# Optimization experiments

Hardware: AMD Instinct MI355X
Metric: run time of the kernel (lower is better)

## Reference

```python
import jax, jax.numpy as jnp
import numpy as np

HIDDEN = 1024
N_HEADS = 16
HEAD_DIM = HIDDEN // N_HEADS  # 64


def setup_inputs() -> dict:
    key = jax.random.key(0)
    ks = jax.random.split(key, 5)
    B, S = 4, 4096
    x = jax.random.normal(ks[0], (B, S, HIDDEN), dtype=jnp.float32)
    scale = 1.0 / np.sqrt(HIDDEN)
    wq = jax.random.normal(ks[1], (HIDDEN, HIDDEN), dtype=jnp.float32) * scale
    wk = jax.random.normal(ks[2], (HIDDEN, HIDDEN), dtype=jnp.float32) * scale
    wv = jax.random.normal(ks[3], (HIDDEN, HIDDEN), dtype=jnp.float32) * scale
    wo = jax.random.normal(ks[4], (HIDDEN, HIDDEN), dtype=jnp.float32) * scale
    return {"x": x, "wq": wq, "wk": wk, "wv": wv, "wo": wo}


def reference(x, wq, wk, wv, wo):
    # Weights stored as (out, in) like torch nn.Linear; y = x @ W^T
    B, S, H = x.shape
    q = (x @ wq.T).reshape(B, S, N_HEADS, HEAD_DIM)
    k = (x @ wk.T).reshape(B, S, N_HEADS, HEAD_DIM)
    v = (x @ wv.T).reshape(B, S, N_HEADS, HEAD_DIM)
    # Faithful to original: no transpose to (B,H,S,D) -> scores are over HEADS
    # attn: (B, S, H_heads, H_heads)
    attn = jnp.einsum("bshd,bsgd->bshg", q, k) / np.sqrt(HEAD_DIM)
    attn = jax.nn.softmax(attn, axis=-1)
    out = jnp.einsum("bshg,bsgd->bshd", attn, v).reshape(B, S, H)
    return out @ wo.T
```

## Files before the change

### kernel.cpp

```cpp
#include <hip/hip_runtime.h>
#include <hip/hip_bf16.h>


typedef __bf16 bf16;
typedef __attribute__((ext_vector_type(8))) __bf16 bf16x8;
typedef __attribute__((ext_vector_type(4))) float floatx4;

#define HIDDEN 1024
#define BM 128
#define BN 128
#define BK 32

#define VMCNT(N) asm volatile("s_waitcnt vmcnt(" #N ")" ::: "memory")
#define LGKM0()                                                                \
    do {                                                                       \
        asm volatile("s_waitcnt lgkmcnt(0)" ::: "memory");                     \
        __builtin_amdgcn_sched_barrier(0);                                     \
    } while (0)
#define SBAR() __builtin_amdgcn_s_barrier()

__device__ __forceinline__ void async_load16(const bf16* g, bf16* lds) {
    __builtin_amdgcn_global_load_lds(
        (const __attribute__((address_space(1))) void*)g,
        (__attribute__((address_space(3))) void*)lds, 16, 0, 0);
}

__device__ __forceinline__ bf16x8 load8(const bf16* p) {
    return *(const bf16x8*)p;
}
__device__ __forceinline__ bf16x8 load8(const float* p) {
    floatx4 lo = *(const floatx4*)p;
    floatx4 hi = *(const floatx4*)(p + 4);
    bf16x8 r;
#pragma unroll
    for (int i = 0; i < 4; ++i) { r[i] = (bf16)lo[i]; r[i + 4] = (bf16)hi[i]; }
    return r;
}

__global__ __launch_bounds__(256) void cvt_all(
    const float* __restrict__ x,
    const float* __restrict__ wq, const float* __restrict__ wk,
    const float* __restrict__ wv, const float* __restrict__ wo,
    bf16* __restrict__ xb, bf16* __restrict__ wpk, int mh8)
{
    const int per = (HIDDEN * HIDDEN) / 8;
    int i = blockIdx.x * 256 + threadIdx.x;
    if (i < mh8) {
        *(bf16x8*)&xb[(size_t)i * 8] = load8(&x[(size_t)i * 8]);
    } else {
        int j = i - mh8;
        int wsel = j / per;
        int off  = (j - wsel * per) * 8;
        const float* s = wsel == 0 ? wq : wsel == 1 ? wk : wsel == 2 ? wv : wo;
        *(bf16x8*)&wpk[(size_t)j * 8] = load8(&s[off]);
    }
}


template <int S>
__device__ __forceinline__ void stage_half(const bf16* __restrict__ gbase,
                                           int ld, int kt, bf16* lhalf,
                                           int h, int tid) {
#pragma unroll
    for (int j = 0; j < 2; ++j) {
        const int ci = j * 512 + tid;
        const int rr = ci >> 3;
        const int cs = (ci & 7) ^ (rr & 7);
        const int gr = h * S + (rr & (S - 1)) + (rr >> (S == 64 ? 6 : 5)) * (2 * S);
        async_load16(&gbase[(size_t)gr * ld + kt + cs * 8], &lhalf[ci * 8]);
    }
}

__device__ __forceinline__ void ld_a4(const bf16* h, int wm, int col, int quad,
                                      int cx, bf16x8* a) {
#pragma unroll
    for (int i = 0; i < 4; ++i) {
        const int rr = i * 16 + col + (wm << 6);
#pragma unroll
        for (int kk = 0; kk < 2; ++kk)
            a[i * 2 + kk] =
                *(const bf16x8*)&h[rr * 64 + (((kk << 2) + quad) ^ cx) * 8];
    }
}
__device__ __forceinline__ void ld_b2(const bf16* h, int wn, int col, int quad,
                                      int cx, bf16x8* b) {
#pragma unroll
    for (int j = 0; j < 2; ++j) {
        const int rr = j * 16 + col + (wn << 5);
#pragma unroll
        for (int kk = 0; kk < 2; ++kk)
            b[j * 2 + kk] =
                *(const bf16x8*)&h[rr * 64 + (((kk << 2) + quad) ^ cx) * 8];
    }
}

template <int H, int G>
__device__ __forceinline__ void mmq(floatx4 (&acc)[8][4], const bf16x8 (&a)[8],
                                    const bf16x8 (&bb)[4]) {
    __builtin_amdgcn_s_setprio(1);
#pragma unroll
    for (int i = 0; i < 4; ++i)
#pragma unroll
        for (int j = 0; j < 2; ++j)
#pragma unroll
            for (int kk = 0; kk < 2; ++kk)
                acc[H * 4 + i][G * 2 + j] =
                    __builtin_amdgcn_mfma_f32_16x16x32_bf16(
                        a[i * 2 + kk], bb[j * 2 + kk],
                        acc[H * 4 + i][G * 2 + j], 0, 0, 0);
    __builtin_amdgcn_s_setprio(0);
}

template <typename TC>
__global__ __launch_bounds__(512, 2) void gemm8p(
    const bf16* __restrict__ A, const bf16* __restrict__ W,
    TC* __restrict__ C, int K, int lda, int ldc)
{
    __shared__ __align__(16) bf16 sA[2][2][128 * 64];
    __shared__ __align__(16) bf16 sB[2][2][128 * 64];

    const int tid  = threadIdx.x;
    const int lane = tid & 63;
    const int w    = tid >> 6;
    const int wm   = w >> 2;
    const int wn   = w & 3;
    const int col  = lane & 15;
    const int quad = lane >> 4;
    const int cx   = col & 7;

    const int gx = gridDim.x, gy = gridDim.y;
    const int nwg = gx * gy;
    int lin = blockIdx.y * gx + blockIdx.x;
    if ((nwg & 7) == 0) {
        const int cpx = nwg >> 3;
        lin = (lin & 7) * cpx + (lin >> 3);
    }
    const int m0 = (lin / gy) * 256;
    const int n0 = (lin % gy) * 256;

    const bf16* Ab = A + (size_t)m0 * lda;
    const bf16* Wb = W + (size_t)n0 * K;

    floatx4 acc[8][4] = {};
    bf16x8 a[8], b0[4], b1[4];

    const int T = K / 64;

    stage_half<64>(Ab, lda, 0, sA[0][0], 0, tid);
    stage_half<32>(Wb, K,   0, sB[0][0], 0, tid);
    stage_half<32>(Wb, K,   0, sB[0][1], 1, tid);
    stage_half<64>(Ab, lda, 0, sA[0][1], 1, tid);
    if (T > 1) {
        stage_half<64>(Ab, lda, 64, sA[1][0], 0, tid);
        stage_half<32>(Wb, K,   64, sB[1][0], 0, tid);
        stage_half<32>(Wb, K,   64, sB[1][1], 1, tid);
        VMCNT(6);
    } else {
        VMCNT(0);
    }
    SBAR();

    for (int t = 0; t < T; ++t) {
        const int b = t & 1;

        ld_a4(sA[b][0], wm, col, quad, cx, a);
        ld_b2(sB[b][0], wn, col, quad, cx, b0);
        if (t + 1 < T) stage_half<64>(Ab, lda, (t + 1) * 64, sA[b ^ 1][1], 1, tid);
        SBAR();
        LGKM0();
        mmq<0, 0>(acc, a, b0);
        SBAR();

        ld_b2(sB[b][1], wn, col, quad, cx, b1);
        SBAR();
        LGKM0();
        mmq<0, 1>(acc, a, b1);
        SBAR();

        ld_a4(sA[b][1], wm, col, quad, cx, a);
        if (t + 2 < T) {
            stage_half<64>(Ab, lda, (t + 2) * 64, sA[b][0], 0, tid);
            stage_half<32>(Wb, K,   (t + 2) * 64, sB[b][0], 0, tid);
        }
        SBAR();
        LGKM0();
        mmq<1, 1>(acc, a, b1);
        SBAR();

        if (t + 2 < T) {
            stage_half<32>(Wb, K, (t + 2) * 64, sB[b][1], 1, tid);
            VMCNT(6);
        } else {
            VMCNT(0);
        }
        SBAR();
        LGKM0();
        mmq<1, 0>(acc, a, b0);
        SBAR();
    }

#pragma unroll
    for (int mi = 0; mi < 8; ++mi) {
#pragma unroll
        for (int r = 0; r < 4; ++r) {
            const int row = m0 + wm * 128 + mi * 16 + quad * 4 + r;
#pragma unroll
            for (int ni = 0; ni < 4; ++ni) {
                const int cc = n0 + wn * 64 + ni * 16 + col;
                C[(size_t)row * ldc + cc] = (TC)acc[mi][ni][r];
            }
        }
    }
}

template <typename TA, typename TB, typename TC>
__global__ __launch_bounds__(256, 2) void gemm_bt(
    const TA* __restrict__ A, const TB* __restrict__ W,
    TC* __restrict__ C, int M, int N, int K)
{
    __shared__ __align__(16) bf16 sA[BM * BK];
    __shared__ __align__(16) bf16 sB[BN * BK];

    const int tid  = threadIdx.x;
    const int lane = tid & 63;
    const int w    = tid >> 6;
    const int wm   = w >> 1;
    const int wn   = w & 1;
    const int m0   = blockIdx.x * BM;
    const int n0   = blockIdx.y * BN;
    const int col  = lane & 15;
    const int quad = lane >> 4;

    floatx4 acc[4][4] = {};

    for (int kt = 0; kt < K; kt += BK) {
        bf16x8 ga[2], gb[2];
#pragma unroll
        for (int i = 0; i < 2; ++i) {
            const int c   = i * 256 + tid;
            const int row = c >> 2;
            const int kc  = c & 3;
            ga[i] = load8(&A[(size_t)(m0 + row) * K + kt + kc * 8]);
            gb[i] = load8(&W[(size_t)(n0 + row) * K + kt + kc * 8]);
        }
        __syncthreads();
#pragma unroll
        for (int i = 0; i < 2; ++i) {
            const int c = i * 256 + tid;
            *(bf16x8*)&sA[c * 8] = ga[i];
            *(bf16x8*)&sB[c * 8] = gb[i];
        }
        __syncthreads();

        bf16x8 af[4], bfr[4];
#pragma unroll
        for (int mi = 0; mi < 4; ++mi)
            af[mi] = *(const bf16x8*)&sA[(wm * 64 + mi * 16 + col) * BK + quad * 8];
#pragma unroll
        for (int ni = 0; ni < 4; ++ni)
            bfr[ni] = *(const bf16x8*)&sB[(wn * 64 + ni * 16 + col) * BK + quad * 8];

#pragma unroll
        for (int mi = 0; mi < 4; ++mi)
#pragma unroll
            for (int ni = 0; ni < 4; ++ni)
                acc[mi][ni] = __builtin_amdgcn_mfma_f32_16x16x32_bf16(
                    af[mi], bfr[ni], acc[mi][ni], 0, 0, 0);
    }

#pragma unroll
    for (int mi = 0; mi < 4; ++mi) {
#pragma unroll
        for (int r = 0; r < 4; ++r) {
            const int row = m0 + wm * 64 + mi * 16 + quad * 4 + r;
#pragma unroll
            for (int ni = 0; ni < 4; ++ni) {
                const int cc = n0 + wn * 64 + ni * 16 + col;
                C[(size_t)row * N + cc] = (TC)acc[mi][ni][r];
            }
        }
    }
}

__global__ __launch_bounds__(256) void attn_heads(
    bf16* base, size_t koff, size_t voff, int stride, bf16* ob)
{
    __shared__ __align__(16) bf16 sP[4][16 * 40];

    const int tid   = threadIdx.x;
    const int lane  = tid & 63;
    const int w     = tid >> 6;
    const int token = blockIdx.x * 4 + w;
    const int col   = lane & 15;
    const int quad  = lane >> 4;

    bf16* qt = base + (size_t)token * stride;
    const bf16* kt = qt + koff;
    const bf16* vt = qt + voff;
    bf16* ot = ob + (size_t)token * HIDDEN;

    bf16x8 vb[4] = {};
    if (quad < 2) {
#pragma unroll
        for (int dt = 0; dt < 4; ++dt)
#pragma unroll
            for (int j = 0; j < 8; ++j)
                vb[dt][j] = vt[(quad * 8 + j) * 64 + dt * 16 + col];
    }

    bf16x8 qa0 = *(const bf16x8*)&qt[col * 64 + quad * 8];
    bf16x8 qa1 = *(const bf16x8*)&qt[col * 64 + 32 + quad * 8];
    bf16x8 kb0 = *(const bf16x8*)&kt[col * 64 + quad * 8];
    bf16x8 kb1 = *(const bf16x8*)&kt[col * 64 + 32 + quad * 8];
    floatx4 s = {};
    s = __builtin_amdgcn_mfma_f32_16x16x32_bf16(qa0, kb0, s, 0, 0, 0);
    s = __builtin_amdgcn_mfma_f32_16x16x32_bf16(qa1, kb1, s, 0, 0, 0);

#pragma unroll
    for (int r = 0; r < 4; ++r) {
        float e = __expf(s[r] * 0.125f);
        float su = e;
#pragma unroll
        for (int off = 1; off < 16; off <<= 1)
            su += __shfl_xor(su, off);
        sP[w][(quad * 4 + r) * 40 + col] = (bf16)(e / su);
    }

    bf16x8 pa = {};
    if (quad < 2) pa = *(const bf16x8*)&sP[w][col * 40 + quad * 8];
#pragma unroll
    for (int dt = 0; dt < 4; ++dt) {
        floatx4 o4 = {};
        o4 = __builtin_amdgcn_mfma_f32_16x16x32_bf16(pa, vb[dt], o4, 0, 0, 0);
#pragma unroll
        for (int r = 0; r < 4; ++r)
            ot[(quad * 4 + r) * 64 + dt * 16 + col] = (bf16)o4[r];
    }
}

extern "C" void kernel_launch(void* const* d_in, const int* in_sizes, int n_in,
                              void* d_out, int out_size, void* d_ws, size_t ws_size,
                              hipStream_t stream) {
    const float* x  = (const float*)d_in[0];
    const float* wq = (const float*)d_in[1];
    const float* wk = (const float*)d_in[2];
    const float* wv = (const float*)d_in[3];
    const float* wo = (const float*)d_in[4];
    float* out = (float*)d_out;

    const int M = in_sizes[0] / HIDDEN;
    const size_t MH = (size_t)M * HIDDEN;
    const size_t WH = (size_t)HIDDEN * HIDDEN;

    const size_t need = (MH + 4 * WH + (size_t)M * 3 * HIDDEN) * sizeof(bf16);

    if (ws_size >= need && (M % 256) == 0) {
        bf16* xb  = (bf16*)d_ws;
        bf16* wpk = xb + MH;
        bf16* qkv = wpk + 4 * WH;

        const int mh8 = (int)(MH / 8);
        const int nchunks = mh8 + (int)(4 * WH / 8);
        cvt_all<<<dim3(nchunks / 256), 256, 0, stream>>>(x, wq, wk, wv, wo,
                                                         xb, wpk, mh8);

        gemm8p<bf16><<<dim3(M / 256, 3 * HIDDEN / 256), 512, 0, stream>>>(
            xb, wpk, qkv, HIDDEN, HIDDEN, 3 * HIDDEN);

        attn_heads<<<dim3(M / 4), 256, 0, stream>>>(qkv, 1024, 2048,
                                                    3 * HIDDEN, xb);

        gemm8p<float><<<dim3(M / 256, HIDDEN / 256), 512, 0, stream>>>(
            xb, wpk + 3 * WH, out, HIDDEN, HIDDEN, HIDDEN);
    } else {
        bf16* qb = (bf16*)d_ws;
        bf16* kb = qb + MH;
        bf16* vb = kb + MH;
        dim3 grid(M / BM, HIDDEN / BN), block(256);
        gemm_bt<float, float, bf16><<<grid, block, 0, stream>>>(x, wq, qb, M, HIDDEN, HIDDEN);
        gemm_bt<float, float, bf16><<<grid, block, 0, stream>>>(x, wk, kb, M, HIDDEN, HIDDEN);
        gemm_bt<float, float, bf16><<<grid, block, 0, stream>>>(x, wv, vb, M, HIDDEN, HIDDEN);
        attn_heads<<<dim3(M / 4), block, 0, stream>>>(qb, MH, 2 * MH, HIDDEN, qb);
        gemm_bt<bf16, float, float><<<grid, block, 0, stream>>>(qb, wo, out, M, HIDDEN, HIDDEN);
    }
}
```

Baseline: 291.4 us.

## Restructure GEMM warp tiling and epilogue, stage attention loads through LDS

The GEMM now loads the whole A tile into registers once per k-step and cycles four W fragments through it. Its prefetch moves from two stages ahead to one, and the grid-swizzle block remapping is removed. The bf16 output path is transposed through LDS for coalesced 8-byte stores, and the fp32 path writes float4 vectors. The attention kernel stages Q/K/V through swizzled LDS with async loads and writes its output via LDS as coalesced vector stores, replacing scalar strided global accesses. Removing the swizzle and the shallower prefetch may reduce L2 reuse and latency hiding.

```diff
diff --git a/kernel.cpp b/kernel.cpp
--- a/kernel.cpp
+++ b/kernel.cpp
@@ -71,43 +71,40 @@
     }
 }
 
-__device__ __forceinline__ void ld_a4(const bf16* h, int wm, int col, int quad,
-                                      int cx, bf16x8* a) {
-#pragma unroll
-    for (int i = 0; i < 4; ++i) {
-        const int rr = i * 16 + col + (wm << 6);
+__device__ __forceinline__ void ld_x8(const bf16* h, int wmh, int col, int quad,
+                                      int cx, bf16x8 (&xf)[4][2]) {
+#pragma unroll
+    for (int ni = 0; ni < 4; ++ni) {
+        const int rr = wmh * 64 + ni * 16 + col;
 #pragma unroll
         for (int kk = 0; kk < 2; ++kk)
-            a[i * 2 + kk] =
-                *(const bf16x8*)&h[rr * 64 + (((kk << 2) + quad) ^ cx) * 8];
-    }
-}
-__device__ __forceinline__ void ld_b2(const bf16* h, int wn, int col, int quad,
-                                      int cx, bf16x8* b) {
-#pragma unroll
-    for (int j = 0; j < 2; ++j) {
-        const int rr = j * 16 + col + (wn << 5);
+            xf[ni][kk] = *(const bf16x8*)&h[rr * 64 + (((kk << 2) + quad) ^ cx) * 8];
+    }
+}
+__device__ __forceinline__ void ld_w2(const bf16* h, int rbase, int col, int quad,
+                                      int cx, bf16x8 (&wf)[2][2]) {
+#pragma unroll
+    for (int i = 0; i < 2; ++i) {
+        const int rr = rbase + i * 16 + col;
 #pragma unroll
         for (int kk = 0; kk < 2; ++kk)
-            b[j * 2 + kk] =
-                *(const bf16x8*)&h[rr * 64 + (((kk << 2) + quad) ^ cx) * 8];
-    }
-}
-
-template <int H, int G>
-__device__ __forceinline__ void mmq(floatx4 (&acc)[8][4], const bf16x8 (&a)[8],
-                                    const bf16x8 (&bb)[4]) {
+            wf[i][kk] = *(const bf16x8*)&h[rr * 64 + (((kk << 2) + quad) ^ cx) * 8];
+    }
+}
+
+template <int P>
+__device__ __forceinline__ void mmqp(floatx4 (&acc)[8][4],
+                                     const bf16x8 (&wf)[2][2],
+                                     const bf16x8 (&xf)[4][2]) {
     __builtin_amdgcn_s_setprio(1);
 #pragma unroll
-    for (int i = 0; i < 4; ++i)
-#pragma unroll
-        for (int j = 0; j < 2; ++j)
+    for (int i = 0; i < 2; ++i)
+#pragma unroll
+        for (int ni = 0; ni < 4; ++ni)
 #pragma unroll
             for (int kk = 0; kk < 2; ++kk)
-                acc[H * 4 + i][G * 2 + j] =
-                    __builtin_amdgcn_mfma_f32_16x16x32_bf16(
-                        a[i * 2 + kk], bb[j * 2 + kk],
-                        acc[H * 4 + i][G * 2 + j], 0, 0, 0);
+                acc[2 * P + i][ni] = __builtin_amdgcn_mfma_f32_16x16x32_bf16(
+                    wf[i][kk], xf[ni][kk], acc[2 * P + i][ni], 0, 0, 0);
     __builtin_amdgcn_s_setprio(0);
 }
 
@@ -116,100 +113,113 @@
     const bf16* __restrict__ A, const bf16* __restrict__ W,
     TC* __restrict__ C, int K, int lda, int ldc)
 {
-    __shared__ __align__(16) bf16 sA[2][2][128 * 64];
-    __shared__ __align__(16) bf16 sB[2][2][128 * 64];
+    __shared__ __align__(16) bf16 smem[65536];
 
     const int tid  = threadIdx.x;
     const int lane = tid & 63;
     const int w    = tid >> 6;
-    const int wm   = w >> 2;
-    const int wn   = w & 3;
+    const int wm4  = w & 3;
+    const int wn2  = w >> 2;
     const int col  = lane & 15;
     const int quad = lane >> 4;
     const int cx   = col & 7;
 
-    const int gx = gridDim.x, gy = gridDim.y;
-    const int nwg = gx * gy;
-    int lin = blockIdx.y * gx + blockIdx.x;
-    if ((nwg & 7) == 0) {
-        const int cpx = nwg >> 3;
-        lin = (lin & 7) * cpx + (lin >> 3);
-    }
-    const int m0 = (lin / gy) * 256;
-    const int n0 = (lin % gy) * 256;
+    const int m0 = blockIdx.x * 256;
+    const int n0 = blockIdx.y * 256;
+
+    bf16* sAp[2][2], *sBp[2][2];
+#pragma unroll
+    for (int b = 0; b < 2; ++b)
+#pragma unroll
+        for (int h = 0; h < 2; ++h) {
+            sAp[b][h] = smem + (b * 2 + h) * 8192;
+            sBp[b][h] = smem + 32768 + (b * 2 + h) * 8192;
+        }
 
     const bf16* Ab = A + (size_t)m0 * lda;
     const bf16* Wb = W + (size_t)n0 * K;
 
     floatx4 acc[8][4] = {};
-    bf16x8 a[8], b0[4], b1[4];
-
-    const int T = K / 64;
-
-    stage_half<64>(Ab, lda, 0, sA[0][0], 0, tid);
-    stage_half<32>(Wb, K,   0, sB[0][0], 0, tid);
-    stage_half<32>(Wb, K,   0, sB[0][1], 1, tid);
-    stage_half<64>(Ab, lda, 0, sA[0][1], 1, tid);
-    if (T > 1) {
-        stage_half<64>(Ab, lda, 64, sA[1][0], 0, tid);
-        stage_half<32>(Wb, K,   64, sB[1][0], 0, tid);
-        stage_half<32>(Wb, K,   64, sB[1][1], 1, tid);
-        VMCNT(6);
-    } else {
-        VMCNT(0);
-    }
+    bf16x8 xf[4][2], wf[2][2];
+
+    const int hx  = wm4 & 1;
+    const int wmh = wm4 >> 1;
+    const int T   = K / 64;
+
+    stage_half<64>(Ab, lda, 0, sAp[0][0], 0, tid);
+    stage_half<64>(Ab, lda, 0, sAp[0][1], 1, tid);
+    stage_half<32>(Wb, K,   0, sBp[0][0], 0, tid);
+    stage_half<32>(Wb, K,   0, sBp[0][1], 1, tid);
+    VMCNT(2);
     SBAR();
 
     for (int t = 0; t < T; ++t) {
         const int b = t & 1;
-
-        ld_a4(sA[b][0], wm, col, quad, cx, a);
-        ld_b2(sB[b][0], wn, col, quad, cx, b0);
-        if (t + 1 < T) stage_half<64>(Ab, lda, (t + 1) * 64, sA[b ^ 1][1], 1, tid);
+        const int kt1 = (t + 1) * 64;
+
+        ld_x8(sAp[b][hx], wmh, col, quad, cx, xf);
+        ld_w2(sBp[b][0], wn2 * 64, col, quad, cx, wf);
+        if (t + 1 < T) {
+            stage_half<64>(Ab, lda, kt1, sAp[b ^ 1][0], 0, tid);
+            stage_half<64>(Ab, lda, kt1, sAp[b ^ 1][1], 1, tid);
+        }
         SBAR();
         LGKM0();
-        mmq<0, 0>(acc, a, b0);
-        SBAR();
-
-        ld_b2(sB[b][1], wn, col, quad, cx, b1);
+        mmqp<0>(acc, wf, xf);
+        if (t + 1 < T) { VMCNT(4); } else { VMCNT(0); }
+        SBAR();
+
+        ld_w2(sBp[b][1], wn2 * 64, col, quad, cx, wf);
+        if (t + 1 < T) stage_half<32>(Wb, K, kt1, sBp[b ^ 1][0], 0, tid);
         SBAR();
         LGKM0();
-        mmq<0, 1>(acc, a, b1);
-        SBAR();
-
-        ld_a4(sA[b][1], wm, col, quad, cx, a);
-        if (t + 2 < T) {
-            stage_half<64>(Ab, lda, (t + 2) * 64, sA[b][0], 0, tid);
-            stage_half<32>(Wb, K,   (t + 2) * 64, sB[b][0], 0, tid);
-        }
+        mmqp<1>(acc, wf, xf);
+        SBAR();
+
+        ld_w2(sBp[b][0], wn2 * 64 + 32, col, quad, cx, wf);
+        if (t + 1 < T) stage_half<32>(Wb, K, kt1, sBp[b ^ 1][1], 1, tid);
         SBAR();
         LGKM0();
-        mmq<1, 1>(acc, a, b1);
-        SBAR();
-
-        if (t + 2 < T) {
-            stage_half<32>(Wb, K, (t + 2) * 64, sB[b][1], 1, tid);
-            VMCNT(6);
-        } else {
-            VMCNT(0);
-        }
+        mmqp<2>(acc, wf, xf);
+        SBAR();
+
+        ld_w2(sBp[b][1], wn2 * 64 + 32, col, quad, cx, wf);
         SBAR();
         LGKM0();
-        mmq<1, 0>(acc, a, b0);
-        SBAR();
-    }
-
-#pragma unroll
-    for (int mi = 0; mi < 8; ++mi) {
-#pragma unroll
-        for (int r = 0; r < 4; ++r) {
-            const int row = m0 + wm * 128 + mi * 16 + quad * 4 + r;
+        mmqp<3>(acc, wf, xf);
+        VMCNT(2);
+        SBAR();
+    }
+
+    if constexpr (sizeof(TC) == 2) {
+#pragma unroll
+        for (int mi = 0; mi < 8; ++mi)
 #pragma unroll
             for (int ni = 0; ni < 4; ++ni) {
-                const int cc = n0 + wn * 64 + ni * 16 + col;
-                C[(size_t)row * ldc + cc] = (TC)acc[mi][ni][r];
+                union { bf16 h4[4]; uint2 u; } pk;
+#pragma unroll
+                for (int r = 0; r < 4; ++r) pk.h4[r] = (bf16)acc[mi][ni][r];
+                const int ml = wm4 * 64 + ni * 16 + col;
+                const int j  = wn2 * 32 + mi * 4 + quad;
+                *(uint2*)&smem[ml * 256 + (j ^ (ml & 15)) * 4] = pk.u;
             }
-        }
+        __syncthreads();
+#pragma unroll
+        for (int it = 0; it < 32; ++it) {
+            const int m  = it * 8 + w;
+            const int jp = lane ^ (m & 15);
+            const uint2 d = *(const uint2*)&smem[m * 256 + jp * 4];
+            *(uint2*)&C[(size_t)(m0 + m) * ldc + n0 + lane * 4] = d;
+        }
+    } else {
+#pragma unroll
+        for (int mi = 0; mi < 8; ++mi)
+#pragma unroll
+            for (int ni = 0; ni < 4; ++ni) {
+                const int m  = m0 + wm4 * 64 + ni * 16 + col;
+                const int nn = n0 + wn2 * 128 + mi * 16 + quad * 4;
+                *(floatx4*)&C[(size_t)m * ldc + nn] = acc[mi][ni];
+            }
     }
 }
 
@@ -285,7 +295,9 @@
 __global__ __launch_bounds__(256) void attn_heads(
     bf16* base, size_t koff, size_t voff, int stride, bf16* ob)
 {
+    __shared__ __align__(16) bf16 sQ[4][3072];
     __shared__ __align__(16) bf16 sP[4][16 * 40];
+    __shared__ __align__(16) bf16 sO[4][1024];
 
     const int tid   = threadIdx.x;
     const int lane  = tid & 63;
@@ -295,26 +307,44 @@
     const int quad  = lane >> 4;
 
     bf16* qt = base + (size_t)token * stride;
-    const bf16* kt = qt + koff;
-    const bf16* vt = qt + voff;
+    const bf16* src0 = qt;
+    const bf16* src1 = qt + koff;
+    const bf16* src2 = qt + voff;
     bf16* ot = ob + (size_t)token * HIDDEN;
 
-    bf16x8 vb[4] = {};
+#pragma unroll
+    for (int i = 0; i < 6; ++i) {
+        const int ci = i * 64 + lane;
+        const int rl = (ci >> 3) & 15;
+        const int cs = (ci & 7) ^ (rl & 7);
+        const bf16* s = (i < 2) ? src0 : (i < 4) ? src1 : src2;
+        async_load16(&s[(rl * 8 + cs) * 8], &sQ[w][ci * 8]);
+    }
+    VMCNT(0);
+
+    bf16x8 qa[2], kb[2];
+#pragma unroll
+    for (int kk = 0; kk < 2; ++kk) {
+        const int c = ((kk << 2) + quad) ^ (col & 7);
+        qa[kk] = *(const bf16x8*)&sQ[w][(col * 8 + c) * 8];
+        kb[kk] = *(const bf16x8*)&sQ[w][((16 + col) * 8 + c) * 8];
+    }
+    floatx4 s = {};
+    s = __builtin_amdgcn_mfma_f32_16x16x32_bf16(qa[0], kb[0], s, 0, 0, 0);
+    s = __builtin_amdgcn_mfma_f32_16x16x32_bf16(qa[1], kb[1], s, 0, 0, 0);
+
+    bf16x8 va[4] = {};
     if (quad < 2) {
 #pragma unroll
-        for (int dt = 0; dt < 4; ++dt)
-#pragma unroll
-            for (int j = 0; j < 8; ++j)
-                vb[dt][j] = vt[(quad * 8 + j) * 64 + dt * 16 + col];
-    }
-
-    bf16x8 qa0 = *(const bf16x8*)&qt[col * 64 + quad * 8];
-    bf16x8 qa1 = *(const bf16x8*)&qt[col * 64 + 32 + quad * 8];
-    bf16x8 kb0 = *(const bf16x8*)&kt[col * 64 + quad * 8];
-    bf16x8 kb1 = *(const bf16x8*)&kt[col * 64 + 32 + quad * 8];
-    floatx4 s = {};
-    s = __builtin_amdgcn_mfma_f32_16x16x32_bf16(qa0, kb0, s, 0, 0, 0);
-    s = __builtin_amdgcn_mfma_f32_16x16x32_bf16(qa1, kb1, s, 0, 0, 0);
+        for (int dt = 0; dt < 4; ++dt) {
+            const int cb = dt * 2 + (col >> 3);
+#pragma unroll
+            for (int j = 0; j < 8; ++j) {
+                const int r = 32 + quad * 8 + j;
+                va[dt][j] = sQ[w][(r * 8 + (cb ^ j)) * 8 + (col & 7)];
+            }
+        }
+    }
 
 #pragma unroll
     for (int r = 0; r < 4; ++r) {
@@ -331,10 +361,20 @@
 #pragma unroll
     for (int dt = 0; dt < 4; ++dt) {
         floatx4 o4 = {};
-        o4 = __builtin_amdgcn_mfma_f32_16x16x32_bf16(pa, vb[dt], o4, 0, 0, 0);
-#pragma unroll
-        for (int r = 0; r < 4; ++r)
-            ot[(quad * 4 + r) * 64 + dt * 16 + col] = (bf16)o4[r];
+        o4 = __builtin_amdgcn_mfma_f32_16x16x32_bf16(va[dt], pa, o4, 0, 0, 0);
+        union { bf16 h4[4]; uint2 u; } pk;
+#pragma unroll
+        for (int r = 0; r < 4; ++r) pk.h4[r] = (bf16)o4[r];
+        const int c8 = dt * 4 + quad;
+        *(uint2*)&sO[w][(col * 16 + (c8 ^ col)) * 4] = pk.u;
+    }
+
+#pragma unroll
+    for (int it = 0; it < 4; ++it) {
+        const int n8 = it * 64 + lane;
+        const int h = n8 >> 4, c8 = n8 & 15;
+        const uint2 d = *(const uint2*)&sO[w][(h * 16 + (c8 ^ h)) * 4];
+        *(uint2*)&ot[n8 * 4] = d;
     }
 }
 
```

After: 430.4 us. 1.48x slower.
